# Performance work log

Measured on AMD Instinct MI355X. Metric: run time of the kernel, lower is better.

## Reference

```python
import jax, jax.numpy as jnp
import numpy as np

NUM_VOXEL_X = 128
NUM_VOXEL_Y = 128
NUM_CHANNELS = 80


def setup_inputs() -> dict:
    key = jax.random.key(0)
    k1, k2, k3 = jax.random.split(key, 3)
    B, N, D, H, W = 2, 6, 112, 16, 44
    total = B * N * D * H * W
    geom_xyz = jax.random.randint(k1, (total, 3), 0, 128, dtype=jnp.int64 if jax.config.jax_enable_x64 else jnp.int32).astype(jnp.int32)
    depth_features = jax.random.uniform(k2, (total,), dtype=jnp.float32)
    context_features = jax.random.normal(k3, (B, N, NUM_CHANNELS, H, W), dtype=jnp.float32)
    return {
        "geom_xyz": geom_xyz,
        "depth_features": depth_features,
        "context_features": context_features,
        "batch_size": B,
        "num_cams": N,
        "num_depth": D,
        "num_height": H,
        "num_width": W,
    }


def reference(geom_xyz, depth_features, context_features, batch_size, num_cams, num_depth, num_height, num_width):
    B, N, D, H, W = batch_size, num_cams, num_depth, num_height, num_width
    C = NUM_CHANNELS
    total = B * N * D * H * W

    # per-point feature = depth * context (context does not depend on depth bin)
    depth = depth_features.reshape(B, N, D, H, W)
    ctx = jnp.transpose(context_features, (0, 1, 3, 4, 2))  # (B,N,H,W,C)
    feats = depth[..., None] * ctx[:, :, None, :, :, :]      # (B,N,D,H,W,C)
    feats = feats.reshape(total, C)

    x = geom_xyz[:, 0].astype(jnp.int32)
    y = geom_xyz[:, 1].astype(jnp.int32)
    valid = (x >= 0) & (x < NUM_VOXEL_X) & (y >= 0) & (y < NUM_VOXEL_Y)

    batch_idx = (jnp.arange(total, dtype=jnp.int32) // (N * D * H * W))
    flat_idx = batch_idx * (NUM_VOXEL_Y * NUM_VOXEL_X) + jnp.clip(y, 0, NUM_VOXEL_Y - 1) * NUM_VOXEL_X + jnp.clip(x, 0, NUM_VOXEL_X - 1)

    feats = jnp.where(valid[:, None], feats, 0.0)
    out = jax.ops.segment_sum(feats, flat_idx, num_segments=B * NUM_VOXEL_Y * NUM_VOXEL_X)
    return out.reshape(B, NUM_VOXEL_Y, NUM_VOXEL_X, C)
```

## Files before the change

kernel.cpp:

```cpp
#include <hip/hip_runtime.h>


namespace {
constexpr int NVX = 128, NVY = 128, C = 80;
constexpr int B = 2, N = 6, D = 112, H = 16, W = 44;
constexpr int HW    = H * W;
constexpr int BN    = B * N;
constexpr int DHW   = D * HW;
constexpr int NDHW  = N * DHW;
constexpr int TOTAL = B * NDHW;
constexpr int NVOX  = B * NVY * NVX;

constexpr int NBIN  = 512;
constexpr int VPB   = NVOX / NBIN;
constexpr int SLOT  = 8;
constexpr int CAP   = 7;
constexpr int PTS_PER_BLK = 1024;
constexpr int SCAN_BLOCKS = TOTAL / PTS_PER_BLK;
constexpr int TR_BLOCKS   = BN * (C / 16) * (HW / 64);
constexpr int PRE_BLOCKS  = SCAN_BLOCKS + TR_BLOCKS;
constexpr int SPILLCAP = 65536;

constexpr int VCAP = 57;
constexpr int OCAP = 32;
}

__global__ __launch_bounds__(256) void pre_kernel(
    const int*   __restrict__ geom, const float* __restrict__ depth,
    const float* __restrict__ ctx,  float* __restrict__ ctx_t,
    int2* __restrict__ staging, int* __restrict__ spillcnt,
    int2* __restrict__ spill)
{
    __shared__ int2  stage[NBIN * SLOT];
    __shared__ int   bcnt[NBIN];
    __shared__ float tile[16 * 68];

    const int t = threadIdx.x;
    if (blockIdx.x < SCAN_BLOCKS) {
        const int lane = t & 63;
        bcnt[t] = 0; bcnt[t + 256] = 0;
        __syncthreads();

        const int p0 = blockIdx.x * PTS_PER_BLK + t * 4;
        const int4* g4 = (const int4*)(geom + (size_t)3 * p0);
        const int4 q0 = g4[0], q1 = g4[1], q2 = g4[2];
        const float4 dp = *(const float4*)(depth + p0);
        const int xs[4] = {q0.x, q0.w, q1.z, q2.y};
        const int ys[4] = {q0.y, q1.x, q1.w, q2.z};
        const int db[4] = {__float_as_int(dp.x), __float_as_int(dp.y),
                           __float_as_int(dp.z), __float_as_int(dp.w)};

        int bins[4], keys[4], idxv[4];
        #pragma unroll
        for (int u = 0; u < 4; ++u) {
            const int x = xs[u], y = ys[u];
            const bool ok = (unsigned)x < (unsigned)NVX &&
                            (unsigned)y < (unsigned)NVY;
            const int p  = p0 + u;
            const int b  = (p >= NDHW) ? 1 : 0;
            const int v  = (b * NVY + y) * NVX + x;
            const int bn = (unsigned)p / (unsigned)DHW;
            const int hw = (unsigned)p % (unsigned)HW;
            bins[u] = v & 511;
            keys[u] = (v << 14) | (bn * HW + hw);
            idxv[u] = ok ? -1 : -2;
        }
        #pragma unroll
        for (int u = 0; u < 4; ++u)
            if (idxv[u] == -1) idxv[u] = atomicAdd(&bcnt[bins[u]], 1);
        #pragma unroll
        for (int u = 0; u < 4; ++u)
            if ((unsigned)idxv[u] < (unsigned)CAP)
                stage[bins[u] * SLOT + idxv[u]] = make_int2(keys[u], db[u]);
        #pragma unroll
        for (int u = 0; u < 4; ++u) {
            const bool sp = (idxv[u] >= CAP);
            const unsigned long long m = __ballot(sp);
            if (m) {
                const int leader = (int)__ffsll((unsigned long long)m) - 1;
                int base = 0;
                if (lane == leader) base = atomicAdd(spillcnt, (int)__popcll(m));
                base = __shfl(base, leader);
                if (sp) {
                    const int off = base +
                        (int)__popcll(m & ((1ull << lane) - 1ull));
                    if (off < SPILLCAP) spill[off] = make_int2(keys[u], db[u]);
                }
            }
        }
        __syncthreads();
        stage[t * SLOT + CAP].x = bcnt[t];
        stage[(t + 256) * SLOT + CAP].x = bcnt[t + 256];
        __syncthreads();

        const int4* src = (const int4*)stage;
        int4* dst = (int4*)staging;
        #pragma unroll
        for (int k = 0; k < 8; ++k) {
            const int i  = k * 256 + t;
            const int sl = i >> 2, part = i & 3;
            dst[((size_t)sl * SCAN_BLOCKS + blockIdx.x) * 4 + part] = src[i];
        }
    } else {
        const int tb  = blockIdx.x - SCAN_BLOCKS;
        const int bn  = tb / 55;
        const int rem = tb % 55;
        const int c0  = (rem / 11) * 16;
        const int hw0 = (rem % 11) * 64;
        const int cl = t >> 6, hwl = t & 63;
        #pragma unroll
        for (int r = 0; r < 4; ++r) {
            const int c = r * 4 + cl;
            tile[c * 68 + hwl] =
                ctx[(size_t)(bn * C + c0 + c) * HW + hw0 + hwl];
        }
        __syncthreads();
        const int cr = t & 15, hwr = t >> 4;
        #pragma unroll
        for (int r = 0; r < 4; ++r) {
            const int hw = r * 16 + hwr;
            ctx_t[(size_t)(bn * HW + hw0 + hw) * C + c0 + cr] =
                tile[cr * 68 + hw];
        }
    }
}

__global__ __launch_bounds__(1024) void acc_kernel(
    const int2* __restrict__ staging, const float* __restrict__ ctx_t,
    float* __restrict__ out, const int* __restrict__ spillcnt,
    const int2* __restrict__ spill)
{
    __shared__ int2 list[VPB * VCAP];
    __shared__ int  vcnt[VPB];
    __shared__ int  ocnt;
    __shared__ int2 olist[OCAP];

    const int bin  = blockIdx.x;
    const int t    = threadIdx.x;
    const int wave = t >> 6, lane = t & 63;

    if (t < VPB) vcnt[t] = 0;
    if (t == 0) ocnt = 0;
    __syncthreads();

    const int g = lane >> 3, slot = lane & 7;
    constexpr int NCH = (SCAN_BLOCKS + 7) / 8;
    {
        const int s0 = wave * 8 + g;
        int2 e_nxt = make_int2(0, 0);
        if (s0 < SCAN_BLOCKS)
            e_nxt = staging[((size_t)bin * SCAN_BLOCKS + s0) * SLOT + slot];
        for (int c = wave; c < NCH; c += 16) {
            const int2 e = e_nxt;
            const int c2 = c + 16;
            if (c2 < NCH) {
                const int s2 = c2 * 8 + g;
                e_nxt = (s2 < SCAN_BLOCKS)
                    ? staging[((size_t)bin * SCAN_BLOCKS + s2) * SLOT + slot]
                    : make_int2(0, 0);
            }
            const int s = c * 8 + g;
            int cnt = __shfl(e.x, (lane & 56) | CAP);
            cnt = cnt < CAP ? cnt : CAP;
            if (s < SCAN_BLOCKS && slot < cnt) {
                const int vl  = e.x >> 23;
                const int idx = atomicAdd(&vcnt[vl], 1);
                if (idx < VCAP) list[vl * VCAP + idx] = e;
                else { int o = atomicAdd(&ocnt, 1); if (o < OCAP) olist[o] = e; }
            }
        }
    }
    {
        int scnt = *spillcnt;
        scnt = scnt < SPILLCAP ? scnt : SPILLCAP;
        for (int i = t; i < scnt; i += 1024) {
            const int2 e = spill[i];
            if (((e.x >> 14) & 511) == bin) {
                const int vl  = e.x >> 23;
                const int idx = atomicAdd(&vcnt[vl], 1);
                if (idx < VCAP) list[vl * VCAP + idx] = e;
                else { int o = atomicAdd(&ocnt, 1); if (o < OCAP) olist[o] = e; }
            }
        }
    }
    __syncthreads();

    const int off2 = 64 + (lane & 15);
    for (int vv = 0; vv < VPB / 16; ++vv) {
        const int vl = wave * (VPB / 16) + vv;
        int n = vcnt[vl];
        n = n < VCAP ? n : VCAP;
        const int2* lp = list + vl * VCAP;

        float a0 = 0.f, a1 = 0.f, a2 = 0.f, a3 = 0.f;
        float a4 = 0.f, a5 = 0.f, a6 = 0.f, a7 = 0.f;
        float b0 = 0.f, b1 = 0.f, b2 = 0.f, b3 = 0.f;
        float b4 = 0.f, b5 = 0.f, b6 = 0.f, b7 = 0.f;
        int j = 0;
        for (; j + 8 <= n; j += 8) {
            const int2 e0 = lp[j],     e1 = lp[j + 1], e2 = lp[j + 2], e3 = lp[j + 3];
            const int2 e4 = lp[j + 4], e5 = lp[j + 5], e6 = lp[j + 6], e7 = lp[j + 7];
            const float* c0 = ctx_t + (size_t)(e0.x & 16383) * C;
            const float* c1 = ctx_t + (size_t)(e1.x & 16383) * C;
            const float* c2 = ctx_t + (size_t)(e2.x & 16383) * C;
            const float* c3 = ctx_t + (size_t)(e3.x & 16383) * C;
            const float* c4 = ctx_t + (size_t)(e4.x & 16383) * C;
            const float* c5 = ctx_t + (size_t)(e5.x & 16383) * C;
            const float* c6 = ctx_t + (size_t)(e6.x & 16383) * C;
            const float* c7 = ctx_t + (size_t)(e7.x & 16383) * C;
            const float f0 = c0[lane], f1 = c1[lane], f2 = c2[lane], f3 = c3[lane];
            const float f4 = c4[lane], f5 = c5[lane], f6 = c6[lane], f7 = c7[lane];
            const float g0 = c0[off2], g1 = c1[off2], g2 = c2[off2], g3 = c3[off2];
            const float g4 = c4[off2], g5 = c5[off2], g6 = c6[off2], g7 = c7[off2];
            const float w0 = __int_as_float(e0.y), w1 = __int_as_float(e1.y);
            const float w2 = __int_as_float(e2.y), w3 = __int_as_float(e3.y);
            const float w4 = __int_as_float(e4.y), w5 = __int_as_float(e5.y);
            const float w6 = __int_as_float(e6.y), w7 = __int_as_float(e7.y);
            a0 += w0 * f0; a1 += w1 * f1; a2 += w2 * f2; a3 += w3 * f3;
            a4 += w4 * f4; a5 += w5 * f5; a6 += w6 * f6; a7 += w7 * f7;
            b0 += w0 * g0; b1 += w1 * g1; b2 += w2 * g2; b3 += w3 * g3;
            b4 += w4 * g4; b5 += w5 * g5; b6 += w6 * g6; b7 += w7 * g7;
        }
        for (; j + 4 <= n; j += 4) {
            const int2 e0 = lp[j], e1 = lp[j + 1], e2 = lp[j + 2], e3 = lp[j + 3];
            const float* c0 = ctx_t + (size_t)(e0.x & 16383) * C;
            const float* c1 = ctx_t + (size_t)(e1.x & 16383) * C;
            const float* c2 = ctx_t + (size_t)(e2.x & 16383) * C;
            const float* c3 = ctx_t + (size_t)(e3.x & 16383) * C;
            const float f0 = c0[lane], f1 = c1[lane], f2 = c2[lane], f3 = c3[lane];
            const float g0 = c0[off2], g1 = c1[off2], g2 = c2[off2], g3 = c3[off2];
            const float w0 = __int_as_float(e0.y), w1 = __int_as_float(e1.y);
            const float w2 = __int_as_float(e2.y), w3 = __int_as_float(e3.y);
            a0 += w0 * f0; a1 += w1 * f1; a2 += w2 * f2; a3 += w3 * f3;
            b0 += w0 * g0; b1 += w1 * g1; b2 += w2 * g2; b3 += w3 * g3;
        }
        for (; j < n; ++j) {
            const int2 e = lp[j];
            const float* c = ctx_t + (size_t)(e.x & 16383) * C;
            const float w = __int_as_float(e.y);
            a0 += w * c[lane];
            b0 += w * c[off2];
        }
        const float av = ((a0 + a1) + (a2 + a3)) + ((a4 + a5) + (a6 + a7));
        const float bv = ((b0 + b1) + (b2 + b3)) + ((b4 + b5) + (b6 + b7));
        float* o = out + (size_t)((vl << 9) | bin) * C;
        o[lane] = av;
        if (lane < 16) o[64 + lane] = bv;
    }
    __syncthreads();

    if (wave == 0) {
        int oc = ocnt;
        oc = oc < OCAP ? oc : OCAP;
        for (int i = 0; i < oc; ++i) {
            const int2 e = olist[i];
            const int vl = e.x >> 23, row = e.x & 16383;
            const float dep = __int_as_float(e.y);
            const float* c = ctx_t + (size_t)row * C;
            float* o = out + (size_t)((vl << 9) | bin) * C;
            unsafeAtomicAdd(o + lane, dep * c[lane]);
            if (lane < 16) unsafeAtomicAdd(o + 64 + lane, dep * c[64 + lane]);
        }
    }
}

extern "C" void kernel_launch(void* const* d_in, const int* in_sizes, int n_in,
                              void* d_out, int out_size, void* d_ws, size_t ws_size,
                              hipStream_t stream) {
    const int*   geom  = (const int*)d_in[0];
    const float* depth = (const float*)d_in[1];
    const float* ctx   = (const float*)d_in[2];
    float*       out   = (float*)d_out;

    char* ws = (char*)d_ws;
    int2* staging  = (int2*)ws; ws += (size_t)NBIN * SCAN_BLOCKS * SLOT * 8;
    int2* spill    = (int2*)ws; ws += (size_t)SPILLCAP * 8;
    int*  spillcnt = (int*)ws;  ws += 256;
    float* ctx_t   = (float*)ws;

    hipMemsetAsync(spillcnt, 0, 256, stream);

    pre_kernel<<<dim3(PRE_BLOCKS), dim3(256),  0, stream>>>(
                  geom, depth, ctx, ctx_t, staging, spillcnt, spill);
    acc_kernel<<<dim3(NBIN),       dim3(1024), 0, stream>>>(
                  staging, ctx_t, out, spillcnt, spill);
}
```

Baseline: 118.0 us.

## Vectorize per-voxel gather with float4 lanes split across three point groups

The accumulation loop changes from one lane per channel (64 plus 16 lanes for the 80 channels) to 20 lanes per point, each loading a float4 of context. Three points are processed at once per wavefront and combined with shuffles. The aim is to cut the number of gather load instructions and the idle lanes on the 16-channel tail. It also deepens staging prefetch to two chunks ahead and replaces per-point div/mod with incremental index tracking in the scan kernel. Four of the 64 lanes now sit idle, and results need a cross-lane reduction.

```diff
diff --git a/kernel.cpp b/kernel.cpp
--- a/kernel.cpp
+++ b/kernel.cpp
@@ -50,20 +50,25 @@
         const int db[4] = {__float_as_int(dp.x), __float_as_int(dp.y),
                            __float_as_int(dp.z), __float_as_int(dp.w)};
 
+        int bnv = (int)((unsigned)p0 / (unsigned)DHW);
+        int rem = p0 - bnv * DHW;
+        int hwv = rem % HW;
+        const int bb = (blockIdx.x >= SCAN_BLOCKS / 2) ? 1 : 0;
+
         int bins[4], keys[4], idxv[4];
         #pragma unroll
         for (int u = 0; u < 4; ++u) {
             const int x = xs[u], y = ys[u];
             const bool ok = (unsigned)x < (unsigned)NVX &&
                             (unsigned)y < (unsigned)NVY;
-            const int p  = p0 + u;
-            const int b  = (p >= NDHW) ? 1 : 0;
-            const int v  = (b * NVY + y) * NVX + x;
-            const int bn = (unsigned)p / (unsigned)DHW;
-            const int hw = (unsigned)p % (unsigned)HW;
+            const int v   = (bb * NVY + y) * NVX + x;
+            const int row = bnv * HW + hwv;
             bins[u] = v & 511;
-            keys[u] = (v << 14) | (bn * HW + hw);
+            keys[u] = (v << 14) | row;
             idxv[u] = ok ? -1 : -2;
+            ++rem; ++hwv;
+            if (rem == DHW)      { rem = 0; ++bnv; hwv = 0; }
+            else if (hwv == HW)  { hwv = 0; }
         }
         #pragma unroll
         for (int u = 0; u < 4; ++u)
@@ -143,23 +148,22 @@
     if (t == 0) ocnt = 0;
     __syncthreads();
 
-    const int g = lane >> 3, slot = lane & 7;
+    const int g8 = lane >> 3, slot = lane & 7;
     constexpr int NCH = (SCAN_BLOCKS + 7) / 8;
     {
-        const int s0 = wave * 8 + g;
-        int2 e_nxt = make_int2(0, 0);
-        if (s0 < SCAN_BLOCKS)
-            e_nxt = staging[((size_t)bin * SCAN_BLOCKS + s0) * SLOT + slot];
+        auto ldchunk = [&](int c) -> int2 {
+            const int s = c * 8 + g8;
+            return (c < NCH && s < SCAN_BLOCKS)
+                ? staging[((size_t)bin * SCAN_BLOCKS + s) * SLOT + slot]
+                : make_int2(0, 0);
+        };
+        int2 eA = ldchunk(wave);
+        int2 eB = ldchunk(wave + 16);
         for (int c = wave; c < NCH; c += 16) {
-            const int2 e = e_nxt;
-            const int c2 = c + 16;
-            if (c2 < NCH) {
-                const int s2 = c2 * 8 + g;
-                e_nxt = (s2 < SCAN_BLOCKS)
-                    ? staging[((size_t)bin * SCAN_BLOCKS + s2) * SLOT + slot]
-                    : make_int2(0, 0);
-            }
-            const int s = c * 8 + g;
+            const int2 e = eA;
+            eA = eB;
+            eB = ldchunk(c + 32);
+            const int s = c * 8 + g8;
             int cnt = __shfl(e.x, (lane & 56) | CAP);
             cnt = cnt < CAP ? cnt : CAP;
             if (s < SCAN_BLOCKS && slot < cnt) {
@@ -185,67 +189,39 @@
     }
     __syncthreads();
 
-    const int off2 = 64 + (lane & 15);
+    const int g3 = lane / 20;
+    const int p  = lane % 20;
+    const int ch0 = p * 4;
     for (int vv = 0; vv < VPB / 16; ++vv) {
         const int vl = wave * (VPB / 16) + vv;
         int n = vcnt[vl];
         n = n < VCAP ? n : VCAP;
         const int2* lp = list + vl * VCAP;
 
-        float a0 = 0.f, a1 = 0.f, a2 = 0.f, a3 = 0.f;
-        float a4 = 0.f, a5 = 0.f, a6 = 0.f, a7 = 0.f;
-        float b0 = 0.f, b1 = 0.f, b2 = 0.f, b3 = 0.f;
-        float b4 = 0.f, b5 = 0.f, b6 = 0.f, b7 = 0.f;
-        int j = 0;
-        for (; j + 8 <= n; j += 8) {
-            const int2 e0 = lp[j],     e1 = lp[j + 1], e2 = lp[j + 2], e3 = lp[j + 3];
-            const int2 e4 = lp[j + 4], e5 = lp[j + 5], e6 = lp[j + 6], e7 = lp[j + 7];
-            const float* c0 = ctx_t + (size_t)(e0.x & 16383) * C;
-            const float* c1 = ctx_t + (size_t)(e1.x & 16383) * C;
-            const float* c2 = ctx_t + (size_t)(e2.x & 16383) * C;
-            const float* c3 = ctx_t + (size_t)(e3.x & 16383) * C;
-            const float* c4 = ctx_t + (size_t)(e4.x & 16383) * C;
-            const float* c5 = ctx_t + (size_t)(e5.x & 16383) * C;
-            const float* c6 = ctx_t + (size_t)(e6.x & 16383) * C;
-            const float* c7 = ctx_t + (size_t)(e7.x & 16383) * C;
-            const float f0 = c0[lane], f1 = c1[lane], f2 = c2[lane], f3 = c3[lane];
-            const float f4 = c4[lane], f5 = c5[lane], f6 = c6[lane], f7 = c7[lane];
-            const float g0 = c0[off2], g1 = c1[off2], g2 = c2[off2], g3 = c3[off2];
-            const float g4 = c4[off2], g5 = c5[off2], g6 = c6[off2], g7 = c7[off2];
-            const float w0 = __int_as_float(e0.y), w1 = __int_as_float(e1.y);
-            const float w2 = __int_as_float(e2.y), w3 = __int_as_float(e3.y);
-            const float w4 = __int_as_float(e4.y), w5 = __int_as_float(e5.y);
-            const float w6 = __int_as_float(e6.y), w7 = __int_as_float(e7.y);
-            a0 += w0 * f0; a1 += w1 * f1; a2 += w2 * f2; a3 += w3 * f3;
-            a4 += w4 * f4; a5 += w5 * f5; a6 += w6 * f6; a7 += w7 * f7;
-            b0 += w0 * g0; b1 += w1 * g1; b2 += w2 * g2; b3 += w3 * g3;
-            b4 += w4 * g4; b5 += w5 * g5; b6 += w6 * g6; b7 += w7 * g7;
-        }
-        for (; j + 4 <= n; j += 4) {
-            const int2 e0 = lp[j], e1 = lp[j + 1], e2 = lp[j + 2], e3 = lp[j + 3];
-            const float* c0 = ctx_t + (size_t)(e0.x & 16383) * C;
-            const float* c1 = ctx_t + (size_t)(e1.x & 16383) * C;
-            const float* c2 = ctx_t + (size_t)(e2.x & 16383) * C;
-            const float* c3 = ctx_t + (size_t)(e3.x & 16383) * C;
-            const float f0 = c0[lane], f1 = c1[lane], f2 = c2[lane], f3 = c3[lane];
-            const float g0 = c0[off2], g1 = c1[off2], g2 = c2[off2], g3 = c3[off2];
-            const float w0 = __int_as_float(e0.y), w1 = __int_as_float(e1.y);
-            const float w2 = __int_as_float(e2.y), w3 = __int_as_float(e3.y);
-            a0 += w0 * f0; a1 += w1 * f1; a2 += w2 * f2; a3 += w3 * f3;
-            b0 += w0 * g0; b1 += w1 * g1; b2 += w2 * g2; b3 += w3 * g3;
-        }
-        for (; j < n; ++j) {
-            const int2 e = lp[j];
-            const float* c = ctx_t + (size_t)(e.x & 16383) * C;
-            const float w = __int_as_float(e.y);
-            a0 += w * c[lane];
-            b0 += w * c[off2];
-        }
-        const float av = ((a0 + a1) + (a2 + a3)) + ((a4 + a5) + (a6 + a7));
-        const float bv = ((b0 + b1) + (b2 + b3)) + ((b4 + b5) + (b6 + b7));
-        float* o = out + (size_t)((vl << 9) | bin) * C;
-        o[lane] = av;
-        if (lane < 16) o[64 + lane] = bv;
+        float4 s = make_float4(0.f, 0.f, 0.f, 0.f);
+        for (int j = 0; j < n; j += 12) {
+            #pragma unroll
+            for (int k = 0; k < 4; ++k) {
+                const int idx = j + k * 3 + g3;
+                const bool ok = (g3 < 3) && (idx < n);
+                const int2 e = lp[ok ? idx : 0];
+                const float w = ok ? __int_as_float(e.y) : 0.f;
+                const int row = e.x & 16383;
+                const float4 cf =
+                    *(const float4*)(ctx_t + (size_t)row * C + ch0);
+                s.x += w * cf.x; s.y += w * cf.y;
+                s.z += w * cf.z; s.w += w * cf.w;
+            }
+        }
+        float4 r;
+        r.x = s.x + __shfl(s.x, p + 20) + __shfl(s.x, p + 40);
+        r.y = s.y + __shfl(s.y, p + 20) + __shfl(s.y, p + 40);
+        r.z = s.z + __shfl(s.z, p + 20) + __shfl(s.z, p + 40);
+        r.w = s.w + __shfl(s.w, p + 20) + __shfl(s.w, p + 40);
+        if (lane < 20) {
+            float* o = out + (size_t)((vl << 9) | bin) * C;
+            *(float4*)(o + ch0) = r;
+        }
     }
     __syncthreads();
 
```

Measured after the change: 109.0 us. -7.6%, faster.
